# Optimization experiments

Measured on AMD Instinct MI355X. Metric: run time of the kernel, lower is better.

## Reference

```python
import jax, jax.numpy as jnp
import numpy as np

N, E, F, DE, G, C = 50000, 800000, 64, 32, 512, 2
EPS = 1e-5


def setup_inputs() -> dict:
    key = jax.random.key(0)
    ks = jax.random.split(key, 12)
    Z = 2 * F + DE  # CGConv concat dim [x_i, x_j, edge_attr]
    inp = {
        "x": jax.random.normal(ks[0], (N, F), dtype=jnp.float32),
        "edge_index": jax.random.randint(ks[1], (2, E), 0, N, dtype=jnp.int32),
        "edge_attr": jax.random.normal(ks[2], (E, DE), dtype=jnp.float32),
        "batch": jnp.sort(jax.random.randint(ks[3], (N,), 0, G, dtype=jnp.int32)),
        # CGConv lin_f / lin_s : (2F+De) -> F, with bias
        "Wf": jax.random.normal(ks[4], (Z, F), dtype=jnp.float32) * 0.05,
        "bf": jnp.zeros((F,), dtype=jnp.float32),
        "Ws": jax.random.normal(ks[5], (Z, F), dtype=jnp.float32) * 0.05,
        "bs": jnp.zeros((F,), dtype=jnp.float32),
        # CGConv internal BatchNorm (training-mode batch stats)
        "bn_w": jnp.ones((F,), dtype=jnp.float32),
        "bn_b": jnp.zeros((F,), dtype=jnp.float32),
        # PyG LayerNorm (graph mode, batch=None -> whole-tensor stats)
        "ln_w": jnp.ones((F,), dtype=jnp.float32),
        "ln_b": jnp.zeros((F,), dtype=jnp.float32),
        # final linear (2F -> C) and output LayerNorm
        "Wl": jax.random.normal(ks[6], (2 * F, C), dtype=jnp.float32) * 0.05,
        "bl": jnp.zeros((C,), dtype=jnp.float32),
        "ln4_w": jnp.ones((C,), dtype=jnp.float32),
        "ln4_b": jnp.zeros((C,), dtype=jnp.float32),
    }
    return inp


def _pyg_layernorm(x, w, b):
    # torch_geometric.nn.LayerNorm, mode='graph', batch=None: whole-tensor stats
    xc = x - jnp.mean(x)
    out = xc / (jnp.sqrt(jnp.mean(xc * xc)) + EPS)
    return out * w + b


def reference(x, edge_index, edge_attr, batch, Wf, bf, Ws, bs, bn_w, bn_b,
              ln_w, ln_b, Wl, bl, ln4_w, ln4_b):
    src = edge_index[0]  # x_j (source)
    dst = edge_index[1]  # x_i (target / aggregation index)

    # CGConv message: sigmoid(lin_f(z)) * softplus(lin_s(z)), z=[x_i,x_j,e]
    z = jnp.concatenate([x[dst], x[src], edge_attr], axis=1)  # [E, 2F+De]
    msg = jax.nn.sigmoid(z @ Wf + bf) * jax.nn.softplus(z @ Ws + bs)  # [E,F]

    # scatter-add aggregation to target nodes
    agg = jax.ops.segment_sum(msg, dst, num_segments=N)  # [N,F]

    # CGConv batch_norm=True (training-mode batch statistics over nodes)
    mu = jnp.mean(agg, axis=0)
    var = jnp.mean((agg - mu) ** 2, axis=0)
    agg = (agg - mu) / jnp.sqrt(var + EPS) * bn_w + bn_b

    # residual
    h = agg + x

    # LayerNorm + softplus
    h = jax.nn.softplus(_pyg_layernorm(h, ln_w, ln_b))

    # global mean / add pooling over graphs
    add_pool = jax.ops.segment_sum(h, batch, num_segments=G)  # [G,F]
    counts = jax.ops.segment_sum(jnp.ones((N,), h.dtype), batch, num_segments=G)
    mean_pool = add_pool / jnp.maximum(counts, 1.0)[:, None]

    g = jnp.concatenate([mean_pool, add_pool], axis=1)  # [G, 2F]
    out = g @ Wl + bl  # [G, C]
    out = _pyg_layernorm(out, ln4_w, ln4_b)
    return out
```

## Files before the change

### kernel.cpp

```cpp
#include <hip/hip_runtime.h>
#include <math.h>

#define EPSF 1e-5f

typedef short bf16x8 __attribute__((ext_vector_type(8)));
typedef float f32x4 __attribute__((ext_vector_type(4)));

static __device__ __forceinline__ unsigned short f2bf(float x) {
  unsigned u = __float_as_uint(x);
  unsigned r = (u + 0x7FFFu + ((u >> 16) & 1u)) >> 16;
  return (unsigned short)r;
}

__global__ __launch_bounds__(256) void node_gemm(
    const float* __restrict__ x, const float* __restrict__ Wf,
    const float* __restrict__ bf, const float* __restrict__ Ws,
    const float* __restrict__ bs, float* __restrict__ Pdst,
    float* __restrict__ Psrc, int N) {
  const int lane = threadIdx.x & 63;
  const int w = threadIdx.x >> 6;
  const float* W = (w & 1) ? Ws : Wf;
  const int baseRow = (w >> 1) * 64;
  float wreg[64];
#pragma unroll
  for (int k = 0; k < 64; ++k) wreg[k] = W[(baseRow + k) * 64 + lane];
  float bias = 0.f;
  if (w == 0) bias = bf[lane];
  if (w == 1) bias = bs[lane];
  float* outp = (w >> 1) ? Psrc : Pdst;
  const int outOff = (w & 1) * 64;

  for (int n = blockIdx.x; n < N; n += gridDim.x) {
    const float* xr = x + (size_t)n * 64;
    float acc = bias;
#pragma unroll
    for (int k = 0; k < 64; k += 4) {
      float4 xv = *(const float4*)(xr + k);
      acc = fmaf(xv.x, wreg[k], acc);
      acc = fmaf(xv.y, wreg[k + 1], acc);
      acc = fmaf(xv.z, wreg[k + 2], acc);
      acc = fmaf(xv.w, wreg[k + 3], acc);
    }
    outp[(size_t)n * 128 + outOff + lane] = acc;
  }
}

__global__ __launch_bounds__(512) void bfrag_kernel(
    const float* __restrict__ Wf, const float* __restrict__ Ws,
    unsigned short* __restrict__ Bfrag) {
  const int l = threadIdx.x & 63, t8 = threadIdx.x >> 6;
  const int q = l & 15, g = l >> 4;
  const float* W = (t8 < 4) ? Wf : Ws;
  const int col = (t8 & 3) * 16 + q;
  unsigned short out[8];
#pragma unroll
  for (int i = 0; i < 8; ++i)
    out[i] = f2bf(W[(size_t)(128 + g * 8 + i) * 64 + col]);
  *(uint4*)&Bfrag[((size_t)t8 * 64 + l) * 8] = *(uint4*)out;
}

__global__ void hist_kernel(const int* __restrict__ ei, int* __restrict__ deg,
                            int E) {
  int i = blockIdx.x * blockDim.x + threadIdx.x;
  if (i < E) atomicAdd(&deg[ei[E + i]], 1);
}

__global__ __launch_bounds__(256) void scan_a(const int* __restrict__ deg,
                                              int* __restrict__ bsum, int N) {
  const int idx = blockIdx.x * 256 + threadIdx.x;
  int v = (idx < N) ? deg[idx] : 0;
#pragma unroll
  for (int o = 32; o > 0; o >>= 1) v += __shfl_down(v, o);
  __shared__ int ws4[4];
  if ((threadIdx.x & 63) == 0) ws4[threadIdx.x >> 6] = v;
  __syncthreads();
  if (threadIdx.x == 0) bsum[blockIdx.x] = ws4[0] + ws4[1] + ws4[2] + ws4[3];
}

__global__ __launch_bounds__(256) void scan_b(const int* __restrict__ bsum,
                                              int* __restrict__ bpre, int NB) {
  const int t = threadIdx.x;
  const int lane = t & 63, w = t >> 6;
  int v = (t < NB) ? bsum[t] : 0;
  int sc = v;
#pragma unroll
  for (int o = 1; o < 64; o <<= 1) {
    int u = __shfl_up(sc, o);
    if (lane >= o) sc += u;
  }
  __shared__ int wsum[4];
  if (lane == 63) wsum[w] = sc;
  __syncthreads();
  int add = 0;
#pragma unroll
  for (int k = 0; k < 4; ++k) add += (k < w) ? wsum[k] : 0;
  bpre[t] = (sc - v) + add;
}

__global__ __launch_bounds__(256) void scan_c(const int* __restrict__ deg,
                                              const int* __restrict__ bpre,
                                              int* __restrict__ offsets,
                                              int* __restrict__ cursor, int N) {
  const int t = threadIdx.x;
  const int lane = t & 63, w = t >> 6;
  const int idx = blockIdx.x * 256 + t;
  int d = (idx < N) ? deg[idx] : 0;
  int sc = d;
#pragma unroll
  for (int o = 1; o < 64; o <<= 1) {
    int u = __shfl_up(sc, o);
    if (lane >= o) sc += u;
  }
  __shared__ int wsum[4];
  if (lane == 63) wsum[w] = sc;
  __syncthreads();
  int add = bpre[blockIdx.x];
#pragma unroll
  for (int k = 0; k < 4; ++k) add += (k < w) ? wsum[k] : 0;
  const int off = add + (sc - d);
  if (idx < N) {
    offsets[idx] = off;
    cursor[idx] = off;
    if (idx == N - 1) offsets[N] = off + d;
  }
}

__global__ void scatter_kernel(const int* __restrict__ ei,
                               int* __restrict__ cursor,
                               int4* __restrict__ epair4, int E) {
  int i = blockIdx.x * blockDim.x + threadIdx.x;
  if (i < E) {
    int dst = ei[E + i];
    int pos = atomicAdd(&cursor[dst], 1);
    epair4[pos] = make_int4(i, ei[i], dst, 0);
  }
}

__global__ __launch_bounds__(256) void edge_mfma(
    const int4* __restrict__ epair4, const float* __restrict__ eattr,
    const unsigned short* __restrict__ Bfrag, const float* __restrict__ Pdst,
    const float* __restrict__ Psrc, float* __restrict__ agg, int E, int N) {
  __shared__ __align__(16) unsigned short Ash[64 * 40];
  __shared__ __align__(16) int sd[128];
  __shared__ int eidx[64];
  __shared__ __align__(4) unsigned char ridb[64];
  __shared__ int rdst[64];
  __shared__ int nruns_s;
  __shared__ float msum[64][66];

  const int t = threadIdx.x, lane = t & 63, w = t >> 6;
  const int q = lane & 15, g = lane >> 4;
  const int base = blockIdx.x * 64;

  if (w == 0) {
    const int eg = base + lane;
    int4 p = make_int4(0, 0, 0, 0);
    if (eg < E) p = epair4[eg];
    const int valid = (eg < E);
    sd[lane * 2] = valid ? p.y : 0;
    sd[lane * 2 + 1] = valid ? p.z : 0;
    eidx[lane] = valid ? p.x : 0;
    int d = valid ? p.z : 0x7FFFFFFF;
    int dprev = __shfl_up(d, 1);
    int flag = (lane == 0 || d != dprev) ? 1 : 0;
    int sc = flag;
#pragma unroll
    for (int o = 1; o < 64; o <<= 1) {
      int u = __shfl_up(sc, o);
      if (lane >= o) sc += u;
    }
    int rid = sc - 1;
    ridb[lane] = (unsigned char)rid;
    if (flag) rdst[rid] = d;
    if (lane == 63) nruns_s = sc;
  }
  for (int i = t; i < 64 * 66; i += 256) ((float*)msum)[i] = 0.f;
  __syncthreads();

  {
    const int row = t >> 2, c = t & 3;
    const float* er = eattr + (size_t)eidx[row] * 32 + c * 8;
    float4 v0 = *(const float4*)er;
    float4 v1 = *(const float4*)(er + 4);
    bf16x8 sv;
    sv[0] = (short)f2bf(v0.x); sv[1] = (short)f2bf(v0.y);
    sv[2] = (short)f2bf(v0.z); sv[3] = (short)f2bf(v0.w);
    sv[4] = (short)f2bf(v1.x); sv[5] = (short)f2bf(v1.y);
    sv[6] = (short)f2bf(v1.z); sv[7] = (short)f2bf(v1.w);
    *(bf16x8*)&Ash[row * 40 + c * 8] = sv;
  }
  __syncthreads();

  union U { uint4 u; bf16x8 v; };
  bf16x8 b[8];
#pragma unroll
  for (int i = 0; i < 8; ++i) {
    U uu;
    uu.u = ((const uint4*)Bfrag)[i * 64 + lane];
    b[i] = uu.v;
  }
  const bf16x8 a = *(const bf16x8*)&Ash[(q + 16 * w) * 40 + g * 8];
  f32x4 acc[8];
#pragma unroll
  for (int i = 0; i < 8; ++i) {
    f32x4 z = {0.f, 0.f, 0.f, 0.f};
    acc[i] = __builtin_amdgcn_mfma_f32_16x16x32_bf16(a, b[i], z, 0, 0, 0);
  }

  const int e0 = 16 * w + g * 4;
  int4 lo = *(const int4*)&sd[e0 * 2];
  int4 hi = *(const int4*)&sd[e0 * 2 + 4];
  const unsigned rid4 = *(const unsigned*)&ridb[e0];
  const float* pdp[4] = {Pdst + (size_t)lo.y * 128, Pdst + (size_t)lo.w * 128,
                         Pdst + (size_t)hi.y * 128, Pdst + (size_t)hi.w * 128};
  const float* psp[4] = {Psrc + (size_t)lo.x * 128, Psrc + (size_t)lo.z * 128,
                         Psrc + (size_t)hi.x * 128, Psrc + (size_t)hi.z * 128};
  const int r0 = rid4 & 255, r1 = (rid4 >> 8) & 255, r2 = (rid4 >> 16) & 255,
            r3 = (rid4 >> 24) & 255;

#pragma unroll
  for (int t8 = 0; t8 < 4; ++t8) {
    const int feat = t8 * 16 + q;
    float mm[4];
#pragma unroll
    for (int reg = 0; reg < 4; ++reg) {
      float Ff = acc[t8][reg] + pdp[reg][feat] + psp[reg][feat];
      float Fs = acc[t8 + 4][reg] + pdp[reg][64 + feat] + psp[reg][64 + feat];
      float sig = __builtin_amdgcn_rcpf(1.0f + __expf(-Ff));
      float sp = fmaxf(Fs, 0.f) + __logf(1.0f + __expf(-fabsf(Fs)));
      mm[reg] = sig * sp;
    }
    float a_ = mm[0];
    int cur = r0;
    if (r1 == cur) a_ += mm[1];
    else { atomicAdd(&msum[cur][feat], a_); cur = r1; a_ = mm[1]; }
    if (r2 == cur) a_ += mm[2];
    else { atomicAdd(&msum[cur][feat], a_); cur = r2; a_ = mm[2]; }
    if (r3 == cur) a_ += mm[3];
    else { atomicAdd(&msum[cur][feat], a_); cur = r3; a_ = mm[3]; }
    atomicAdd(&msum[cur][feat], a_);
  }
  __syncthreads();

  const int nr = nruns_s;
  for (int r = w; r < nr; r += 4) {
    const int dn = rdst[r];
    if (dn < N) atomicAdd(&agg[(size_t)dn * 64 + lane], msum[r][lane]);
  }
}

__global__ __launch_bounds__(256) void stats_kernel(
    const float* __restrict__ agg, const float* __restrict__ x,
    float* __restrict__ stats, int N) {
  const int f = threadIdx.x & 63;
  const int sub = threadIdx.x >> 6;
  float sa = 0, sa2 = 0, sx = 0, sx2 = 0, sax = 0;
  for (int r = blockIdx.x * 4 + sub; r < N; r += gridDim.x * 4) {
    float a = agg[(size_t)r * 64 + f];
    float xv = x[(size_t)r * 64 + f];
    sa += a; sa2 += a * a; sx += xv; sx2 += xv * xv; sax += a * xv;
  }
  __shared__ float lds[4][5][64];
  lds[sub][0][f] = sa; lds[sub][1][f] = sa2; lds[sub][2][f] = sx;
  lds[sub][3][f] = sx2; lds[sub][4][f] = sax;
  __syncthreads();
  if (sub == 0) {
#pragma unroll
    for (int i = 0; i < 5; ++i) {
      float v = lds[0][i][f] + lds[1][i][f] + lds[2][i][f] + lds[3][i][f];
      atomicAdd(&stats[i * 64 + f], v);
    }
  }
}

__global__ __launch_bounds__(64) void finalize_stats(
    const float* __restrict__ stats, const float* __restrict__ bn_w,
    const float* __restrict__ bn_b, float* __restrict__ ab, int N) {
  const int f = threadIdx.x;
  const float Nf = (float)N;
  const float invN = 1.0f / Nf;
  float Sa = stats[f], Sa2 = stats[64 + f], Sx = stats[128 + f],
        Sx2 = stats[192 + f], Sax = stats[256 + f];
  float mu = Sa * invN;
  float var = Sa2 * invN - mu * mu;
  float alpha = bn_w[f] / sqrtf(var + EPSF);
  float beta = bn_b[f] - mu * alpha;
  float Sh = alpha * Sa + Nf * beta + Sx;
  float Sh2 = alpha * alpha * Sa2 + Sx2 + Nf * beta * beta +
              2.f * alpha * Sax + 2.f * alpha * beta * Sa + 2.f * beta * Sx;
#pragma unroll
  for (int o = 32; o > 0; o >>= 1) {
    Sh += __shfl_down(Sh, o);
    Sh2 += __shfl_down(Sh2, o);
  }
  ab[f] = alpha;
  ab[64 + f] = beta;
  if (f == 0) {
    float cnt = Nf * 64.0f;
    float mean = Sh / cnt;
    float msq = Sh2 / cnt - mean * mean;
    ab[128] = mean;
    ab[129] = 1.0f / (sqrtf(fmaxf(msq, 0.f)) + EPSF);
  }
}

__global__ __launch_bounds__(256) void node_finish(
    const float* __restrict__ agg, const float* __restrict__ x,
    const int* __restrict__ batch, const float* __restrict__ ab,
    const float* __restrict__ ln_w, const float* __restrict__ ln_b,
    float* __restrict__ add_pool, float* __restrict__ counts, int N,
    int chunk) {
  const int f = threadIdx.x & 63;
  const int sub = threadIdx.x >> 6;
  const int r0 = blockIdx.x * chunk;
  const int r1 = min(N, r0 + chunk);
  const float alpha = ab[f], beta = ab[64 + f];
  const float mean = ab[128], rden = ab[129];
  const float lw = ln_w[f] * rden;
  const float lb = ln_b[f];
  float acc = 0.f, cacc = 0.f;
  int curg = -1;
  for (int r = r0 + sub; r < r1; r += 4) {
    int g = batch[r];
    if (g != curg) {
      if (curg >= 0) {
        atomicAdd(&add_pool[(size_t)curg * 64 + f], acc);
        if (f == 0) atomicAdd(&counts[curg], cacc);
      }
      curg = g; acc = 0.f; cacc = 0.f;
    }
    float h = fmaf(alpha, agg[(size_t)r * 64 + f], beta) + x[(size_t)r * 64 + f];
    float v = (h - mean) * lw + lb;
    float sp = fmaxf(v, 0.f) + __logf(1.0f + __expf(-fabsf(v)));
    acc += sp; cacc += 1.f;
  }
  if (curg >= 0) {
    atomicAdd(&add_pool[(size_t)curg * 64 + f], acc);
    if (f == 0) atomicAdd(&counts[curg], cacc);
  }
}

__global__ __launch_bounds__(1024) void graph_out(
    const float* __restrict__ add_pool, const float* __restrict__ counts,
    const float* __restrict__ Wl, const float* __restrict__ bl,
    const float* __restrict__ w4, const float* __restrict__ b4,
    float* __restrict__ out, int G) {
  const int t = threadIdx.x;
  const int g = t >> 1, c = t & 1;
  float cnt = fmaxf(counts[g], 1.0f);
  float inv = 1.0f / cnt;
  const float* ap = add_pool + (size_t)g * 64;
  float v = bl[c];
#pragma unroll 8
  for (int k = 0; k < 64; ++k)
    v = fmaf(ap[k], fmaf(Wl[k * 2 + c], inv, Wl[(64 + k) * 2 + c]), v);

  __shared__ float red[16];
  __shared__ float bc[2];
  float sum = v;
#pragma unroll
  for (int o = 32; o > 0; o >>= 1) sum += __shfl_down(sum, o);
  if ((t & 63) == 0) red[t >> 6] = sum;
  __syncthreads();
  if (t == 0) {
    float tot = 0;
#pragma unroll
    for (int i = 0; i < 16; ++i) tot += red[i];
    bc[0] = tot * (1.0f / 1024.0f);
  }
  __syncthreads();
  const float mean = bc[0];
  const float xc = v - mean;
  float sq = xc * xc;
  __syncthreads();
#pragma unroll
  for (int o = 32; o > 0; o >>= 1) sq += __shfl_down(sq, o);
  if ((t & 63) == 0) red[t >> 6] = sq;
  __syncthreads();
  if (t == 0) {
    float tot = 0;
#pragma unroll
    for (int i = 0; i < 16; ++i) tot += red[i];
    bc[1] = 1.0f / (sqrtf(tot * (1.0f / 1024.0f)) + EPSF);
  }
  __syncthreads();
  out[t] = xc * bc[1] * w4[c] + b4[c];
}

extern "C" void kernel_launch(void* const* d_in, const int* in_sizes, int n_in,
                              void* d_out, int out_size, void* d_ws,
                              size_t ws_size, hipStream_t stream) {
  const float* x = (const float*)d_in[0];
  const int* ei = (const int*)d_in[1];
  const float* eattr = (const float*)d_in[2];
  const int* batch = (const int*)d_in[3];
  const float* Wf = (const float*)d_in[4];
  const float* bf = (const float*)d_in[5];
  const float* Ws = (const float*)d_in[6];
  const float* bs = (const float*)d_in[7];
  const float* bn_w = (const float*)d_in[8];
  const float* bn_b = (const float*)d_in[9];
  const float* ln_w = (const float*)d_in[10];
  const float* ln_b = (const float*)d_in[11];
  const float* Wl = (const float*)d_in[12];
  const float* bl = (const float*)d_in[13];
  const float* w4 = (const float*)d_in[14];
  const float* b4 = (const float*)d_in[15];

  const int N = in_sizes[0] / 64;
  const int E = in_sizes[2] / 32;
  const int G = 512;
  const int NB = (N + 255) / 256;
  const int T = (E + 63) / 64;

  float* ws = (float*)d_ws;
  float* agg = ws;
  int* offsets = (int*)(agg + (size_t)N * 64);
  float* stats = (float*)(offsets + N + 4);
  float* add_pool = stats + 320;
  float* counts = add_pool + (size_t)G * 64;
  int* deg = (int*)(counts + G);
  int* cursor = deg + N;
  float* ab = (float*)(cursor + N);
  int* bsum = (int*)(ab + 132);
  int* bpre = bsum + 256;
  unsigned short* Bfrag = (unsigned short*)(bpre + 256);
  int4* epair4 = (int4*)((int*)(bpre + 256) + 2048);
  float* Pdst = (float*)((int*)epair4 + 4 * (size_t)E);
  float* Psrc = Pdst + (size_t)N * 128;

  size_t zeroFloats =
      (size_t)N * 64 + (N + 4) + 320 + (size_t)G * 64 + G + N;
  hipMemsetAsync(agg, 0, zeroFloats * sizeof(float), stream);

  node_gemm<<<1024, 256, 0, stream>>>(x, Wf, bf, Ws, bs, Pdst, Psrc, N);
  bfrag_kernel<<<1, 512, 0, stream>>>(Wf, Ws, Bfrag);
  hist_kernel<<<(E + 255) / 256, 256, 0, stream>>>(ei, deg, E);
  scan_a<<<NB, 256, 0, stream>>>(deg, bsum, N);
  scan_b<<<1, 256, 0, stream>>>(bsum, bpre, NB);
  scan_c<<<NB, 256, 0, stream>>>(deg, bpre, offsets, cursor, N);
  scatter_kernel<<<(E + 255) / 256, 256, 0, stream>>>(ei, cursor, epair4, E);
  edge_mfma<<<T, 256, 0, stream>>>(epair4, eattr, Bfrag, Pdst, Psrc, agg, E, N);
  stats_kernel<<<512, 256, 0, stream>>>(agg, x, stats, N);
  finalize_stats<<<1, 64, 0, stream>>>(stats, bn_w, bn_b, ab, N);
  const int chunk = (N + 511) / 512;
  node_finish<<<512, 256, 0, stream>>>(agg, x, batch, ab, ln_w, ln_b, add_pool,
                                       counts, N, chunk);
  graph_out<<<1, 1024, 0, stream>>>(add_pool, counts, Wl, bl, w4, b4,
                                    (float*)d_out, G);
}
```

Before: 332.5 us.

## Fuse node projections into edge MFMA kernel and merge stats finalize

Removes the per-node projection GEMM (Pdst/Psrc) and instead gathers x[dst] and x[src] per edge, converts them to bf16 in shared memory, and runs the full K=160 MFMA per edge tile. Segmented partial sums now go straight to global atomics, replacing the shared-memory msum staging. The finalize_stats kernel is folded into node_finish, and graph_out gets vectorized loads. This drops two launches and the large Pdst/Psrc round trip, at the cost of more per-edge MFMA work, bf16 rounding of the x inputs, and potentially more global atomics.

```diff
diff --git a/kernel.cpp b/kernel.cpp
--- a/kernel.cpp
+++ b/kernel.cpp
@@ -12,51 +12,24 @@
   return (unsigned short)r;
 }
 
-__global__ __launch_bounds__(256) void node_gemm(
-    const float* __restrict__ x, const float* __restrict__ Wf,
-    const float* __restrict__ bf, const float* __restrict__ Ws,
-    const float* __restrict__ bs, float* __restrict__ Pdst,
-    float* __restrict__ Psrc, int N) {
-  const int lane = threadIdx.x & 63;
-  const int w = threadIdx.x >> 6;
-  const float* W = (w & 1) ? Ws : Wf;
-  const int baseRow = (w >> 1) * 64;
-  float wreg[64];
-#pragma unroll
-  for (int k = 0; k < 64; ++k) wreg[k] = W[(baseRow + k) * 64 + lane];
-  float bias = 0.f;
-  if (w == 0) bias = bf[lane];
-  if (w == 1) bias = bs[lane];
-  float* outp = (w >> 1) ? Psrc : Pdst;
-  const int outOff = (w & 1) * 64;
-
-  for (int n = blockIdx.x; n < N; n += gridDim.x) {
-    const float* xr = x + (size_t)n * 64;
-    float acc = bias;
-#pragma unroll
-    for (int k = 0; k < 64; k += 4) {
-      float4 xv = *(const float4*)(xr + k);
-      acc = fmaf(xv.x, wreg[k], acc);
-      acc = fmaf(xv.y, wreg[k + 1], acc);
-      acc = fmaf(xv.z, wreg[k + 2], acc);
-      acc = fmaf(xv.w, wreg[k + 3], acc);
-    }
-    outp[(size_t)n * 128 + outOff + lane] = acc;
-  }
-}
-
-__global__ __launch_bounds__(512) void bfrag_kernel(
+union BU { uint4 u; bf16x8 v; };
+
+__global__ __launch_bounds__(512) void bpack_kernel(
     const float* __restrict__ Wf, const float* __restrict__ Ws,
     unsigned short* __restrict__ Bfrag) {
-  const int l = threadIdx.x & 63, t8 = threadIdx.x >> 6;
+  const int ks = blockIdx.x;
+  const int t8 = threadIdx.x >> 6, l = threadIdx.x & 63;
   const int q = l & 15, g = l >> 4;
   const float* W = (t8 < 4) ? Wf : Ws;
   const int col = (t8 & 3) * 16 + q;
   unsigned short out[8];
 #pragma unroll
-  for (int i = 0; i < 8; ++i)
-    out[i] = f2bf(W[(size_t)(128 + g * 8 + i) * 64 + col]);
-  *(uint4*)&Bfrag[((size_t)t8 * 64 + l) * 8] = *(uint4*)out;
+  for (int i = 0; i < 8; ++i) {
+    int r = ks * 32 + g * 8 + i;
+    int wr = (r < 32) ? (128 + r) : (r - 32);
+    out[i] = f2bf(W[(size_t)wr * 64 + col]);
+  }
+  *(uint4*)&Bfrag[((size_t)(ks * 8 + t8) * 64 + l) * 8] = *(uint4*)out;
 }
 
 __global__ void hist_kernel(const int* __restrict__ ei, int* __restrict__ deg,
@@ -136,31 +109,42 @@
   }
 }
 
-__global__ __launch_bounds__(256) void edge_mfma(
+__global__ __launch_bounds__(256) void edge_fused(
     const int4* __restrict__ epair4, const float* __restrict__ eattr,
-    const unsigned short* __restrict__ Bfrag, const float* __restrict__ Pdst,
-    const float* __restrict__ Psrc, float* __restrict__ agg, int E, int N) {
-  __shared__ __align__(16) unsigned short Ash[64 * 40];
-  __shared__ __align__(16) int sd[128];
-  __shared__ int eidx[64];
+    const float* __restrict__ x, const unsigned short* __restrict__ Bfrag,
+    const float* __restrict__ bfv_, const float* __restrict__ bsv_,
+    float* __restrict__ agg, int E, int N) {
+  __shared__ __align__(16) unsigned short Ash[5][64][40];
+  __shared__ __align__(16) int srcl[64];
+  __shared__ __align__(16) int dstl[64];
+  __shared__ __align__(16) int eidx[64];
   __shared__ __align__(4) unsigned char ridb[64];
-  __shared__ int rdst[64];
-  __shared__ int nruns_s;
-  __shared__ float msum[64][66];
 
   const int t = threadIdx.x, lane = t & 63, w = t >> 6;
   const int q = lane & 15, g = lane >> 4;
   const int base = blockIdx.x * 64;
 
+  bf16x8 Bf[5], Bs[5];
+#pragma unroll
+  for (int ks = 0; ks < 5; ++ks) {
+    BU u1, u2;
+    u1.u = ((const uint4*)Bfrag)[(size_t)((ks * 8 + w) * 64 + lane)];
+    u2.u = ((const uint4*)Bfrag)[(size_t)((ks * 8 + w + 4) * 64 + lane)];
+    Bf[ks] = u1.v;
+    Bs[ks] = u2.v;
+  }
+  const int feat = w * 16 + q;
+  const float bfv = bfv_[feat];
+  const float bsv = bsv_[feat];
+
   if (w == 0) {
     const int eg = base + lane;
-    int4 p = make_int4(0, 0, 0, 0);
+    int4 p = make_int4(0, 0, 0x7FFFFFFF, 0);
     if (eg < E) p = epair4[eg];
-    const int valid = (eg < E);
-    sd[lane * 2] = valid ? p.y : 0;
-    sd[lane * 2 + 1] = valid ? p.z : 0;
-    eidx[lane] = valid ? p.x : 0;
-    int d = valid ? p.z : 0x7FFFFFFF;
+    eidx[lane] = p.x;
+    srcl[lane] = p.y;
+    dstl[lane] = p.z;
+    int d = p.z;
     int dprev = __shfl_up(d, 1);
     int flag = (lane == 0 || d != dprev) ? 1 : 0;
     int sc = flag;
@@ -169,17 +153,18 @@
       int u = __shfl_up(sc, o);
       if (lane >= o) sc += u;
     }
-    int rid = sc - 1;
-    ridb[lane] = (unsigned char)rid;
-    if (flag) rdst[rid] = d;
-    if (lane == 63) nruns_s = sc;
-  }
-  for (int i = t; i < 64 * 66; i += 256) ((float*)msum)[i] = 0.f;
+    ridb[lane] = (unsigned char)(sc - 1);
+  }
   __syncthreads();
 
   {
     const int row = t >> 2, c = t & 3;
-    const float* er = eattr + (size_t)eidx[row] * 32 + c * 8;
+    const int ei_ = eidx[row];
+    int d_ = dstl[row];
+    if (d_ >= N) d_ = 0;
+    const int s_ = srcl[row];
+
+    const float* er = eattr + (size_t)ei_ * 32 + c * 8;
     float4 v0 = *(const float4*)er;
     float4 v1 = *(const float4*)(er + 4);
     bf16x8 sv;
@@ -187,65 +172,96 @@
     sv[2] = (short)f2bf(v0.z); sv[3] = (short)f2bf(v0.w);
     sv[4] = (short)f2bf(v1.x); sv[5] = (short)f2bf(v1.y);
     sv[6] = (short)f2bf(v1.z); sv[7] = (short)f2bf(v1.w);
-    *(bf16x8*)&Ash[row * 40 + c * 8] = sv;
-  }
-  __syncthreads();
-
-  union U { uint4 u; bf16x8 v; };
-  bf16x8 b[8];
-#pragma unroll
-  for (int i = 0; i < 8; ++i) {
-    U uu;
-    uu.u = ((const uint4*)Bfrag)[i * 64 + lane];
-    b[i] = uu.v;
-  }
-  const bf16x8 a = *(const bf16x8*)&Ash[(q + 16 * w) * 40 + g * 8];
-  f32x4 acc[8];
-#pragma unroll
-  for (int i = 0; i < 8; ++i) {
-    f32x4 z = {0.f, 0.f, 0.f, 0.f};
-    acc[i] = __builtin_amdgcn_mfma_f32_16x16x32_bf16(a, b[i], z, 0, 0, 0);
-  }
-
-  const int e0 = 16 * w + g * 4;
-  int4 lo = *(const int4*)&sd[e0 * 2];
-  int4 hi = *(const int4*)&sd[e0 * 2 + 4];
-  const unsigned rid4 = *(const unsigned*)&ridb[e0];
-  const float* pdp[4] = {Pdst + (size_t)lo.y * 128, Pdst + (size_t)lo.w * 128,
-                         Pdst + (size_t)hi.y * 128, Pdst + (size_t)hi.w * 128};
-  const float* psp[4] = {Psrc + (size_t)lo.x * 128, Psrc + (size_t)lo.z * 128,
-                         Psrc + (size_t)hi.x * 128, Psrc + (size_t)hi.z * 128};
-  const int r0 = rid4 & 255, r1 = (rid4 >> 8) & 255, r2 = (rid4 >> 16) & 255,
-            r3 = (rid4 >> 24) & 255;
-
-#pragma unroll
-  for (int t8 = 0; t8 < 4; ++t8) {
-    const int feat = t8 * 16 + q;
-    float mm[4];
-#pragma unroll
-    for (int reg = 0; reg < 4; ++reg) {
-      float Ff = acc[t8][reg] + pdp[reg][feat] + psp[reg][feat];
-      float Fs = acc[t8 + 4][reg] + pdp[reg][64 + feat] + psp[reg][64 + feat];
-      float sig = __builtin_amdgcn_rcpf(1.0f + __expf(-Ff));
-      float sp = fmaxf(Fs, 0.f) + __logf(1.0f + __expf(-fabsf(Fs)));
-      mm[reg] = sig * sp;
-    }
-    float a_ = mm[0];
-    int cur = r0;
-    if (r1 == cur) a_ += mm[1];
-    else { atomicAdd(&msum[cur][feat], a_); cur = r1; a_ = mm[1]; }
-    if (r2 == cur) a_ += mm[2];
-    else { atomicAdd(&msum[cur][feat], a_); cur = r2; a_ = mm[2]; }
-    if (r3 == cur) a_ += mm[3];
-    else { atomicAdd(&msum[cur][feat], a_); cur = r3; a_ = mm[3]; }
-    atomicAdd(&msum[cur][feat], a_);
-  }
-  __syncthreads();
-
-  const int nr = nruns_s;
-  for (int r = w; r < nr; r += 4) {
-    const int dn = rdst[r];
-    if (dn < N) atomicAdd(&agg[(size_t)dn * 64 + lane], msum[r][lane]);
+    *(bf16x8*)&Ash[0][row][c * 8] = sv;
+
+    const float* xd = x + (size_t)d_ * 64 + c * 16;
+    float4 a0 = *(const float4*)xd;
+    float4 a1 = *(const float4*)(xd + 4);
+    float4 a2 = *(const float4*)(xd + 8);
+    float4 a3 = *(const float4*)(xd + 12);
+    bf16x8 s0, s1;
+    s0[0] = (short)f2bf(a0.x); s0[1] = (short)f2bf(a0.y);
+    s0[2] = (short)f2bf(a0.z); s0[3] = (short)f2bf(a0.w);
+    s0[4] = (short)f2bf(a1.x); s0[5] = (short)f2bf(a1.y);
+    s0[6] = (short)f2bf(a1.z); s0[7] = (short)f2bf(a1.w);
+    s1[0] = (short)f2bf(a2.x); s1[1] = (short)f2bf(a2.y);
+    s1[2] = (short)f2bf(a2.z); s1[3] = (short)f2bf(a2.w);
+    s1[4] = (short)f2bf(a3.x); s1[5] = (short)f2bf(a3.y);
+    s1[6] = (short)f2bf(a3.z); s1[7] = (short)f2bf(a3.w);
+    *(bf16x8*)&Ash[1 + (c >> 1)][row][(c & 1) * 16] = s0;
+    *(bf16x8*)&Ash[1 + (c >> 1)][row][(c & 1) * 16 + 8] = s1;
+
+    const float* xs = x + (size_t)s_ * 64 + c * 16;
+    float4 b0 = *(const float4*)xs;
+    float4 b1 = *(const float4*)(xs + 4);
+    float4 b2 = *(const float4*)(xs + 8);
+    float4 b3 = *(const float4*)(xs + 12);
+    bf16x8 t0, t1;
+    t0[0] = (short)f2bf(b0.x); t0[1] = (short)f2bf(b0.y);
+    t0[2] = (short)f2bf(b0.z); t0[3] = (short)f2bf(b0.w);
+    t0[4] = (short)f2bf(b1.x); t0[5] = (short)f2bf(b1.y);
+    t0[6] = (short)f2bf(b1.z); t0[7] = (short)f2bf(b1.w);
+    t1[0] = (short)f2bf(b2.x); t1[1] = (short)f2bf(b2.y);
+    t1[2] = (short)f2bf(b2.z); t1[3] = (short)f2bf(b2.w);
+    t1[4] = (short)f2bf(b3.x); t1[5] = (short)f2bf(b3.y);
+    t1[6] = (short)f2bf(b3.z); t1[7] = (short)f2bf(b3.w);
+    *(bf16x8*)&Ash[3 + (c >> 1)][row][(c & 1) * 16] = t0;
+    *(bf16x8*)&Ash[3 + (c >> 1)][row][(c & 1) * 16 + 8] = t1;
+  }
+  __syncthreads();
+
+  f32x4 accf[4], accs[4];
+#pragma unroll
+  for (int mt = 0; mt < 4; ++mt) {
+    accf[mt] = (f32x4){0.f, 0.f, 0.f, 0.f};
+    accs[mt] = (f32x4){0.f, 0.f, 0.f, 0.f};
+  }
+#pragma unroll
+  for (int ks = 0; ks < 5; ++ks) {
+#pragma unroll
+    for (int mt = 0; mt < 4; ++mt) {
+      const bf16x8 a = *(const bf16x8*)&Ash[ks][mt * 16 + q][g * 8];
+      accf[mt] =
+          __builtin_amdgcn_mfma_f32_16x16x32_bf16(a, Bf[ks], accf[mt], 0, 0, 0);
+      accs[mt] =
+          __builtin_amdgcn_mfma_f32_16x16x32_bf16(a, Bs[ks], accs[mt], 0, 0, 0);
+    }
+  }
+
+#pragma unroll
+  for (int mt = 0; mt < 4; ++mt) {
+    const int e0 = mt * 16 + g * 4;
+    const unsigned rid4 = *(const unsigned*)&ridb[e0];
+    const int4 d4 = *(const int4*)&dstl[e0];
+    float m[4];
+#pragma unroll
+    for (int r = 0; r < 4; ++r) {
+      float F = accf[mt][r] + bfv;
+      float S = accs[mt][r] + bsv;
+      float sig = __builtin_amdgcn_rcpf(1.0f + __expf(-F));
+      float sp = fmaxf(S, 0.f) + __logf(1.0f + __expf(-fabsf(S)));
+      m[r] = sig * sp;
+    }
+    const int r0 = rid4 & 255, r1 = (rid4 >> 8) & 255, r2 = (rid4 >> 16) & 255,
+              r3 = rid4 >> 24;
+    float a_ = m[0];
+    int cur = r0, dc = d4.x;
+    if (r1 == cur) a_ += m[1];
+    else {
+      if (dc < N) atomicAdd(&agg[(size_t)dc * 64 + feat], a_);
+      cur = r1; dc = d4.y; a_ = m[1];
+    }
+    if (r2 == cur) a_ += m[2];
+    else {
+      if (dc < N) atomicAdd(&agg[(size_t)dc * 64 + feat], a_);
+      cur = r2; dc = d4.z; a_ = m[2];
+    }
+    if (r3 == cur) a_ += m[3];
+    else {
+      if (dc < N) atomicAdd(&agg[(size_t)dc * 64 + feat], a_);
+      cur = r3; dc = d4.w; a_ = m[3];
+    }
+    if (dc < N) atomicAdd(&agg[(size_t)dc * 64 + feat], a_);
   }
 }
 
@@ -273,51 +289,40 @@
   }
 }
 
-__global__ __launch_bounds__(64) void finalize_stats(
+__global__ __launch_bounds__(256) void node_finish(
     const float* __restrict__ stats, const float* __restrict__ bn_w,
-    const float* __restrict__ bn_b, float* __restrict__ ab, int N) {
-  const int f = threadIdx.x;
+    const float* __restrict__ bn_b, const float* __restrict__ agg,
+    const float* __restrict__ x, const int* __restrict__ batch,
+    const float* __restrict__ ln_w, const float* __restrict__ ln_b,
+    float* __restrict__ add_pool, float* __restrict__ counts, int N,
+    int chunk) {
+  const int f = threadIdx.x & 63;
+  const int sub = threadIdx.x >> 6;
   const float Nf = (float)N;
   const float invN = 1.0f / Nf;
   float Sa = stats[f], Sa2 = stats[64 + f], Sx = stats[128 + f],
         Sx2 = stats[192 + f], Sax = stats[256 + f];
   float mu = Sa * invN;
   float var = Sa2 * invN - mu * mu;
-  float alpha = bn_w[f] / sqrtf(var + EPSF);
-  float beta = bn_b[f] - mu * alpha;
+  const float alpha = bn_w[f] / sqrtf(var + EPSF);
+  const float beta = bn_b[f] - mu * alpha;
   float Sh = alpha * Sa + Nf * beta + Sx;
   float Sh2 = alpha * alpha * Sa2 + Sx2 + Nf * beta * beta +
               2.f * alpha * Sax + 2.f * alpha * beta * Sa + 2.f * beta * Sx;
 #pragma unroll
   for (int o = 32; o > 0; o >>= 1) {
-    Sh += __shfl_down(Sh, o);
-    Sh2 += __shfl_down(Sh2, o);
-  }
-  ab[f] = alpha;
-  ab[64 + f] = beta;
-  if (f == 0) {
-    float cnt = Nf * 64.0f;
-    float mean = Sh / cnt;
-    float msq = Sh2 / cnt - mean * mean;
-    ab[128] = mean;
-    ab[129] = 1.0f / (sqrtf(fmaxf(msq, 0.f)) + EPSF);
-  }
-}
-
-__global__ __launch_bounds__(256) void node_finish(
-    const float* __restrict__ agg, const float* __restrict__ x,
-    const int* __restrict__ batch, const float* __restrict__ ab,
-    const float* __restrict__ ln_w, const float* __restrict__ ln_b,
-    float* __restrict__ add_pool, float* __restrict__ counts, int N,
-    int chunk) {
-  const int f = threadIdx.x & 63;
-  const int sub = threadIdx.x >> 6;
+    Sh += __shfl_xor(Sh, o);
+    Sh2 += __shfl_xor(Sh2, o);
+  }
+  const float cnt = Nf * 64.0f;
+  const float mean = Sh / cnt;
+  const float msq = Sh2 / cnt - mean * mean;
+  const float rden = 1.0f / (sqrtf(fmaxf(msq, 0.f)) + EPSF);
+  const float lw = ln_w[f] * rden;
+  const float lb = ln_b[f];
+
   const int r0 = blockIdx.x * chunk;
   const int r1 = min(N, r0 + chunk);
-  const float alpha = ab[f], beta = ab[64 + f];
-  const float mean = ab[128], rden = ab[129];
-  const float lw = ln_w[f] * rden;
-  const float lb = ln_b[f];
   float acc = 0.f, cacc = 0.f;
   int curg = -1;
   for (int r = r0 + sub; r < r1; r += 4) {
@@ -349,11 +354,25 @@
   const int g = t >> 1, c = t & 1;
   float cnt = fmaxf(counts[g], 1.0f);
   float inv = 1.0f / cnt;
-  const float* ap = add_pool + (size_t)g * 64;
+  const float4* ap4 = (const float4*)(add_pool + (size_t)g * 64);
+  const float4* W4 = (const float4*)Wl;
   float v = bl[c];
-#pragma unroll 8
-  for (int k = 0; k < 64; ++k)
-    v = fmaf(ap[k], fmaf(Wl[k * 2 + c], inv, Wl[(64 + k) * 2 + c]), v);
+#pragma unroll 4
+  for (int k4 = 0; k4 < 16; ++k4) {
+    float4 a4 = ap4[k4];
+    float4 wa = W4[k4 * 2];
+    float4 wb = W4[k4 * 2 + 1];
+    float4 wc = W4[32 + k4 * 2];
+    float4 wd = W4[32 + k4 * 2 + 1];
+    float m0 = c ? wa.y : wa.x, m1 = c ? wa.w : wa.z;
+    float m2 = c ? wb.y : wb.x, m3 = c ? wb.w : wb.z;
+    float a0 = c ? wc.y : wc.x, a1 = c ? wc.w : wc.z;
+    float a2 = c ? wd.y : wd.x, a3 = c ? wd.w : wd.z;
+    v = fmaf(a4.x, fmaf(m0, inv, a0), v);
+    v = fmaf(a4.y, fmaf(m1, inv, a1), v);
+    v = fmaf(a4.z, fmaf(m2, inv, a2), v);
+    v = fmaf(a4.w, fmaf(m3, inv, a3), v);
+  }
 
   __shared__ float red[16];
   __shared__ float bc[2];
@@ -415,37 +434,31 @@
 
   float* ws = (float*)d_ws;
   float* agg = ws;
-  int* offsets = (int*)(agg + (size_t)N * 64);
-  float* stats = (float*)(offsets + N + 4);
+  float* stats = agg + (size_t)N * 64;
   float* add_pool = stats + 320;
   float* counts = add_pool + (size_t)G * 64;
   int* deg = (int*)(counts + G);
-  int* cursor = deg + N;
-  float* ab = (float*)(cursor + N);
-  int* bsum = (int*)(ab + 132);
+  int* offsets = deg + N;
+  int* cursor = offsets + N + 4;
+  int* bsum = cursor + N;
   int* bpre = bsum + 256;
   unsigned short* Bfrag = (unsigned short*)(bpre + 256);
-  int4* epair4 = (int4*)((int*)(bpre + 256) + 2048);
-  float* Pdst = (float*)((int*)epair4 + 4 * (size_t)E);
-  float* Psrc = Pdst + (size_t)N * 128;
-
-  size_t zeroFloats =
-      (size_t)N * 64 + (N + 4) + 320 + (size_t)G * 64 + G + N;
+  int4* epair4 = (int4*)((int*)(bpre + 256) + 10240);
+
+  size_t zeroFloats = (size_t)N * 64 + 320 + (size_t)G * 64 + G + N;
   hipMemsetAsync(agg, 0, zeroFloats * sizeof(float), stream);
 
-  node_gemm<<<1024, 256, 0, stream>>>(x, Wf, bf, Ws, bs, Pdst, Psrc, N);
-  bfrag_kernel<<<1, 512, 0, stream>>>(Wf, Ws, Bfrag);
+  bpack_kernel<<<5, 512, 0, stream>>>(Wf, Ws, Bfrag);
   hist_kernel<<<(E + 255) / 256, 256, 0, stream>>>(ei, deg, E);
   scan_a<<<NB, 256, 0, stream>>>(deg, bsum, N);
   scan_b<<<1, 256, 0, stream>>>(bsum, bpre, NB);
   scan_c<<<NB, 256, 0, stream>>>(deg, bpre, offsets, cursor, N);
   scatter_kernel<<<(E + 255) / 256, 256, 0, stream>>>(ei, cursor, epair4, E);
-  edge_mfma<<<T, 256, 0, stream>>>(epair4, eattr, Bfrag, Pdst, Psrc, agg, E, N);
+  edge_fused<<<T, 256, 0, stream>>>(epair4, eattr, x, Bfrag, bf, bs, agg, E, N);
   stats_kernel<<<512, 256, 0, stream>>>(agg, x, stats, N);
-  finalize_stats<<<1, 64, 0, stream>>>(stats, bn_w, bn_b, ab, N);
   const int chunk = (N + 511) / 512;
-  node_finish<<<512, 256, 0, stream>>>(agg, x, batch, ab, ln_w, ln_b, add_pool,
-                                       counts, N, chunk);
+  node_finish<<<512, 256, 0, stream>>>(stats, bn_w, bn_b, agg, x, batch, ln_w,
+                                       ln_b, add_pool, counts, N, chunk);
   graph_out<<<1, 1024, 0, stream>>>(add_pool, counts, Wl, bl, w4, b4,
                                     (float*)d_out, G);
 }
```

After: 334.7 us. No clear change (+0.7%).
